# Kernel tuning notes

Measured on AMD Instinct MI355X. Metric: run time of the kernel, lower is better.

The kernel has to match this reference:

```python
import jax, jax.numpy as jnp
import numpy as np

NQ = 8          # n_qubits
NC = 4          # n_cycles of the angle encoder
PI = np.float32(np.pi)
LAYER_QUBITS = [[0, 1, 2, 3, 4, 5, 6, 7], [1, 3, 5, 7]]  # active qubits per conv layer
FINAL_QUBITS = [3, 7]                                    # active after last pooling
CX = jnp.array([[1, 0, 0, 0], [0, 1, 0, 0], [0, 0, 0, 1], [0, 0, 1, 0]], jnp.complex64)


def apply1(psi, U, q):
    """Apply 1-qubit gate U ((2,2) shared or (B,2,2) batched) on qubit q. psi: (B,2,...,2)."""
    psi = jnp.moveaxis(psi, 1 + q, -1)
    if U.ndim == 3:
        psi = jnp.einsum('bij,b...j->b...i', U, psi)
    else:
        psi = jnp.einsum('ij,...j->...i', U, psi)
    return jnp.moveaxis(psi, -1, 1 + q)


def apply2(psi, U, q0, q1):
    """Apply 2-qubit gate U (4,4) on (q0,q1); q0 is the more-significant wire."""
    psi = jnp.moveaxis(psi, (1 + q0, 1 + q1), (-2, -1))
    sh = psi.shape
    psi = jnp.einsum('ij,...j->...i', U, psi.reshape(sh[:-2] + (4,)))
    return jnp.moveaxis(psi.reshape(sh), (-2, -1), (1 + q0, 1 + q1))


def rz_mat(t):
    return jnp.array([[jnp.exp(-0.5j * t), 0.0], [0.0, jnp.exp(0.5j * t)]]).astype(jnp.complex64)


def ry_mat(t):
    c, s = jnp.cos(t / 2), jnp.sin(t / 2)
    return jnp.array([[c, -s], [s, c]]).astype(jnp.complex64)


def crx_mat(t):
    c = jnp.cos(t / 2).astype(jnp.complex64)
    s = jnp.sin(t / 2).astype(jnp.complex64)
    M = jnp.eye(4, dtype=jnp.complex64)
    return M.at[2, 2].set(c).at[3, 3].set(c).at[2, 3].set(-1j * s).at[3, 2].set(-1j * s)


def u3_mat(t, p, l):
    c, s = jnp.cos(t / 2), jnp.sin(t / 2)
    return jnp.array([[c + 0j, -jnp.exp(1j * l) * s],
                      [jnp.exp(1j * p) * s, jnp.exp(1j * (p + l)) * c]]).astype(jnp.complex64)


def expz(psi, q):
    """<Z_q> = P(q=0) - P(q=1)."""
    p = psi.real ** 2 + psi.imag ** 2
    p = jnp.moveaxis(p, 1 + q, 1).reshape(p.shape[0], 2, -1).sum(-1)
    return p[:, 0] - p[:, 1]


def encode(x):
    """Angle-encoding circuit (circuit_builder): NC cycles of RY(x) + CNOT ring."""
    B = x.shape[0]
    psi = jnp.zeros((B, 2 ** NQ), jnp.complex64).at[:, 0].set(1.0).reshape((B,) + (2,) * NQ)
    for c in range(NC):
        ang = x[:, c * NQ:(c + 1) * NQ]
        cc, ss = jnp.cos(ang / 2), jnp.sin(ang / 2)
        for q in range(NQ):
            U = jnp.stack([jnp.stack([cc[:, q], -ss[:, q]], -1),
                           jnp.stack([ss[:, q], cc[:, q]], -1)], -2).astype(jnp.complex64)
            psi = apply1(psi, U, q)
        for q in range(NQ):
            psi = apply2(psi, CX, q, (q + 1) % NQ)
    return psi


def forward(x, rz_p, ry_p, ry2_p, crx_p, u3_p, u3b_p, W1, b1, W2, b2):
    psi0 = encode(x)
    psi1 = psi0  # deepcopy of encoded state for the second feature map
    for layer in range(2):
        aq = LAYER_QUBITS[layer]
        n = len(aq)
        RZp, RYp, RY2p = rz_mat(rz_p[layer]), ry_mat(ry_p[layer]), ry_mat(ry2_p[layer])
        RZm, RZpl = rz_mat(-PI / 2), rz_mat(PI / 2)
        # circuit 1: ZNOTY-style conv blocks, even pairs then odd pairs
        for parity in (0, 1):
            for i in range(parity, n - 1, 2):
                qc, qt = aq[i], aq[i + 1]
                psi0 = apply1(psi0, RZm, qt)
                psi0 = apply2(psi0, CX, qt, qc)
                psi0 = apply1(psi0, RZp, qc)
                psi0 = apply1(psi0, RYp, qt)
                psi0 = apply2(psi0, CX, qc, qt)
                psi0 = apply1(psi0, RY2p, qt)
                psi0 = apply2(psi0, CX, qt, qc)
                psi0 = apply1(psi0, RZpl, qc)
        remain = [aq[i] for i in range(n) if i % 2 == 1]
        U3a = u3_mat(u3_p[layer, 0], u3_p[layer, 1], u3_p[layer, 2])
        for q in remain:
            psi0 = apply1(psi0, U3a, q)
        # circuit 2: CRX conv blocks, even pairs then odd pairs
        CRXp = crx_mat(crx_p[layer])
        for parity in (0, 1):
            for i in range(parity, n - 1, 2):
                psi1 = apply2(psi1, CRXp, aq[i], aq[i + 1])
        U3b = u3_mat(u3b_p[layer, 0], u3b_p[layer, 1], u3b_p[layer, 2])
        for q in remain:
            psi1 = apply1(psi1, U3b, q)
    xv = jnp.stack([expz(psi0, q) for q in FINAL_QUBITS], 1)  # (B,2)
    yv = jnp.stack([expz(psi1, q) for q in FINAL_QUBITS], 1)  # (B,2)
    feat = jnp.concatenate([xv, yv], 1)                       # (B,4)
    h = jnp.tanh(feat @ W1.T + b1)
    return jax.nn.sigmoid(h @ W2.T + b2)


def setup_inputs() -> dict:
    key = jax.random.key(0)
    ks = jax.random.split(key, 12)
    B = 8192
    return {
        'x': jax.random.normal(ks[0], (B, NC * NQ), jnp.float32),
        'rz_p': jax.random.normal(ks[1], (2,), jnp.float32) * 0.5,
        'ry_p': jax.random.normal(ks[2], (2,), jnp.float32) * 0.5,
        'ry2_p': jax.random.normal(ks[3], (2,), jnp.float32) * 0.5,
        'crx_p': jax.random.normal(ks[4], (2,), jnp.float32) * 0.5,
        'u3_p': jax.random.normal(ks[5], (2, 3), jnp.float32) * 0.5,
        'u3b_p': jax.random.normal(ks[6], (2, 3), jnp.float32) * 0.5,
        'W1': jax.random.normal(ks[7], (15, 4), jnp.float32) * 0.4,
        'b1': jax.random.normal(ks[8], (15,), jnp.float32) * 0.1,
        'W2': jax.random.normal(ks[9], (1, 15), jnp.float32) * 0.25,
        'b2': jax.random.normal(ks[10], (1,), jnp.float32) * 0.1,
    }


def reference(x, rz_p, ry_p, ry2_p, crx_p, u3_p, u3b_p, W1, b1, W2, b2):
    return forward(x, rz_p, ry_p, ry2_p, crx_p, u3_p, u3b_p, W1, b1, W2, b2)
```

## Files before the change

kernel.cpp:

```cpp
#include <hip/hip_runtime.h>

#define DEV __device__ __forceinline__

struct C2 { float r, i; };


template<int P>
DEV void ry_cross(float* pr, float* pi, float gc, float gs, int lane) {
  const float cb = ((lane >> P) & 1) ? gs : -gs;
  #pragma unroll
  for (int s = 0; s < 16; ++s) {
    float br = __shfl_xor(pr[s], 1 << P);
    float bi = __shfl_xor(pi[s], 1 << P);
    pr[s] = gc * pr[s] + cb * br;
    pi[s] = gc * pi[s] + cb * bi;
  }
}

template<int M>
DEV void ry_in(float* pr, float* pi, float gc, float gs) {
  #pragma unroll
  for (int s = 0; s < 16; ++s) if (!(s & M)) {
    const int s1 = s | M;
    float ar = pr[s], ai = pi[s], br = pr[s1], bi = pi[s1];
    pr[s]  = gc * ar - gs * br;  pi[s]  = gc * ai - gs * bi;
    pr[s1] = gs * ar + gc * br;  pi[s1] = gs * ai + gc * bi;
  }
}

template<int PC, int PT>
DEV void cx_cc(float* pr, float* pi, int lane) {
  const bool h = (lane >> PC) & 1;
  #pragma unroll
  for (int s = 0; s < 16; ++s) {
    float tr = __shfl_xor(pr[s], 1 << PT);
    float ti = __shfl_xor(pi[s], 1 << PT);
    pr[s] = h ? tr : pr[s];
    pi[s] = h ? ti : pi[s];
  }
}

template<int PC, int MT>
DEV void cx_ci(float* pr, float* pi, int lane) {
  const bool h = (lane >> PC) & 1;
  #pragma unroll
  for (int s = 0; s < 16; ++s) if (!(s & MT)) {
    const int s1 = s | MT;
    float ar = pr[s], br = pr[s1];
    pr[s] = h ? br : ar;  pr[s1] = h ? ar : br;
    float ai = pi[s], bi = pi[s1];
    pi[s] = h ? bi : ai;  pi[s1] = h ? ai : bi;
  }
}

template<int MC, int MT>
DEV void cx_ii(float* pr, float* pi) {
  #pragma unroll
  for (int s = 0; s < 16; ++s) if ((s & MC) && !(s & MT)) {
    const int s1 = s | MT;
    float t;
    t = pr[s]; pr[s] = pr[s1]; pr[s1] = t;
    t = pi[s]; pi[s] = pi[s1]; pi[s1] = t;
  }
}

template<int MC, int PT>
DEV void cx_ic(float* pr, float* pi) {
  #pragma unroll
  for (int s = 0; s < 16; ++s) if (s & MC) {
    pr[s] = __shfl_xor(pr[s], 1 << PT);
    pi[s] = __shfl_xor(pi[s], 1 << PT);
  }
}


template<int PC, int PT>
DEV void u4_cc(float* pr, float* pi, const float* cw, int lay, int lane) {
  const int bc = (lane >> PC) & 1, bt = (lane >> PT) & 1;
  const int r = (bc << 1) | bt;
  const int base = (lay * 16 + r * 4) * 2;
  const float w0r = cw[base + (r ^ 0) * 2], w0i = cw[base + (r ^ 0) * 2 + 1];
  const float w1r = cw[base + (r ^ 1) * 2], w1i = cw[base + (r ^ 1) * 2 + 1];
  const float w2r = cw[base + (r ^ 2) * 2], w2i = cw[base + (r ^ 2) * 2 + 1];
  const float w3r = cw[base + (r ^ 3) * 2], w3i = cw[base + (r ^ 3) * 2 + 1];
  #pragma unroll
  for (int s = 0; s < 16; ++s) {
    float ar = pr[s], ai = pi[s];
    float tr = __shfl_xor(ar, 1 << PT), ti = __shfl_xor(ai, 1 << PT);
    float cr = __shfl_xor(ar, 1 << PC), ci = __shfl_xor(ai, 1 << PC);
    float ur = __shfl_xor(tr, 1 << PC), ui = __shfl_xor(ti, 1 << PC);
    pr[s] = w0r*ar - w0i*ai + w1r*tr - w1i*ti + w2r*cr - w2i*ci + w3r*ur - w3i*ui;
    pi[s] = w0r*ai + w0i*ar + w1r*ti + w1i*tr + w2r*ci + w2i*cr + w3r*ui + w3i*ur;
  }
}

template<int PC, int MT>
DEV void u4_ci(float* pr, float* pi, const float* cw, int lay, int lane) {
  const int bc = (lane >> PC) & 1;
  const int r0 = bc << 1, r1 = r0 | 1;
  const int b0 = (lay * 16 + r0 * 4) * 2;
  const int b1 = (lay * 16 + r1 * 4) * 2;
  const float A0r = cw[b0 + (r0 ^ 0) * 2], A0i = cw[b0 + (r0 ^ 0) * 2 + 1];
  const float A1r = cw[b0 + (r0 ^ 1) * 2], A1i = cw[b0 + (r0 ^ 1) * 2 + 1];
  const float A2r = cw[b0 + (r0 ^ 2) * 2], A2i = cw[b0 + (r0 ^ 2) * 2 + 1];
  const float A3r = cw[b0 + (r0 ^ 3) * 2], A3i = cw[b0 + (r0 ^ 3) * 2 + 1];
  const float B0r = cw[b1 + (r1 ^ 0) * 2], B0i = cw[b1 + (r1 ^ 0) * 2 + 1];
  const float B1r = cw[b1 + (r1 ^ 1) * 2], B1i = cw[b1 + (r1 ^ 1) * 2 + 1];
  const float B2r = cw[b1 + (r1 ^ 2) * 2], B2i = cw[b1 + (r1 ^ 2) * 2 + 1];
  const float B3r = cw[b1 + (r1 ^ 3) * 2], B3i = cw[b1 + (r1 ^ 3) * 2 + 1];
  #pragma unroll
  for (int s = 0; s < 16; ++s) if (!(s & MT)) {
    const int s1 = s | MT;
    float ar = pr[s], ai = pi[s], br = pr[s1], bi = pi[s1];
    float xar = __shfl_xor(ar, 1 << PC), xai = __shfl_xor(ai, 1 << PC);
    float xbr = __shfl_xor(br, 1 << PC), xbi = __shfl_xor(bi, 1 << PC);
    pr[s]  = A0r*ar - A0i*ai + A1r*br - A1i*bi + A2r*xar - A2i*xai + A3r*xbr - A3i*xbi;
    pi[s]  = A0r*ai + A0i*ar + A1r*bi + A1i*br + A2r*xai + A2i*xar + A3r*xbi + A3i*xbr;
    pr[s1] = B0r*br - B0i*bi + B1r*ar - B1i*ai + B2r*xbr - B2i*xbi + B3r*xar - B3i*xai;
    pi[s1] = B0r*bi + B0i*br + B1r*ai + B1i*ar + B2r*xbi + B2i*xbr + B3r*xai + B3i*xar;
  }
}

template<int MC, int MT>
DEV void u4_ii(float* pr, float* pi, const float* cw, int lay) {
  float u[32];
  #pragma unroll
  for (int k = 0; k < 32; ++k) u[k] = cw[lay * 32 + k];
  #pragma unroll
  for (int s = 0; s < 16; ++s) if (!(s & (MC | MT))) {
    const int s0 = s, s1 = s | MT, s2 = s | MC, s3 = s | MC | MT;
    float v0r = pr[s0], v0i = pi[s0], v1r = pr[s1], v1i = pi[s1];
    float v2r = pr[s2], v2i = pi[s2], v3r = pr[s3], v3i = pi[s3];
    float n0r = u[0]*v0r - u[1]*v0i + u[2]*v1r - u[3]*v1i + u[4]*v2r - u[5]*v2i + u[6]*v3r - u[7]*v3i;
    float n0i = u[0]*v0i + u[1]*v0r + u[2]*v1i + u[3]*v1r + u[4]*v2i + u[5]*v2r + u[6]*v3i + u[7]*v3r;
    float n1r = u[8]*v0r - u[9]*v0i + u[10]*v1r - u[11]*v1i + u[12]*v2r - u[13]*v2i + u[14]*v3r - u[15]*v3i;
    float n1i = u[8]*v0i + u[9]*v0r + u[10]*v1i + u[11]*v1r + u[12]*v2i + u[13]*v2r + u[14]*v3i + u[15]*v3r;
    float n2r = u[16]*v0r - u[17]*v0i + u[18]*v1r - u[19]*v1i + u[20]*v2r - u[21]*v2i + u[22]*v3r - u[23]*v3i;
    float n2i = u[16]*v0i + u[17]*v0r + u[18]*v1i + u[19]*v1r + u[20]*v2i + u[21]*v2r + u[22]*v3i + u[23]*v3r;
    float n3r = u[24]*v0r - u[25]*v0i + u[26]*v1r - u[27]*v1i + u[28]*v2r - u[29]*v2i + u[30]*v3r - u[31]*v3i;
    float n3i = u[24]*v0i + u[25]*v0r + u[26]*v1i + u[27]*v1r + u[28]*v2i + u[29]*v2r + u[30]*v3i + u[31]*v3r;
    pr[s0] = n0r; pi[s0] = n0i; pr[s1] = n1r; pi[s1] = n1i;
    pr[s2] = n2r; pi[s2] = n2i; pr[s3] = n3r; pi[s3] = n3i;
  }
}


DEV void u3_make(float t, float p, float l, C2* u) {
  float c = __cosf(0.5f * t), s = __sinf(0.5f * t);
  float cp = __cosf(p), sp = __sinf(p);
  float cl = __cosf(l), sl = __sinf(l);
  float cpl = __cosf(p + l), spl = __sinf(p + l);
  u[0] = C2{c, 0.0f};
  u[1] = C2{-cl * s, -sl * s};
  u[2] = C2{cp * s, sp * s};
  u[3] = C2{cpl * c, spl * c};
}

template<int P>
DEV void u3_cross(float* pr, float* pi, const C2* u, int lane) {
  const bool h = (lane >> P) & 1;
  const float car = h ? u[3].r : u[0].r, cai = h ? u[3].i : u[0].i;
  const float cbr = h ? u[2].r : u[1].r, cbi = h ? u[2].i : u[1].i;
  #pragma unroll
  for (int s = 0; s < 16; ++s) {
    float br = __shfl_xor(pr[s], 1 << P);
    float bi = __shfl_xor(pi[s], 1 << P);
    float ar = pr[s], ai = pi[s];
    pr[s] = car*ar - cai*ai + cbr*br - cbi*bi;
    pi[s] = car*ai + cai*ar + cbr*bi + cbi*br;
  }
}

template<int M>
DEV void u3_in(float* pr, float* pi, const C2* u) {
  #pragma unroll
  for (int s = 0; s < 16; ++s) if (!(s & M)) {
    const int s1 = s | M;
    float ar = pr[s], ai = pi[s], br = pr[s1], bi = pi[s1];
    pr[s]  = u[0].r*ar - u[0].i*ai + u[1].r*br - u[1].i*bi;
    pi[s]  = u[0].r*ai + u[0].i*ar + u[1].r*bi + u[1].i*br;
    pr[s1] = u[2].r*ar - u[2].i*ai + u[3].r*br - u[3].i*bi;
    pi[s1] = u[2].r*ai + u[2].i*ar + u[3].r*bi + u[3].i*br;
  }
}


template<int PC, int PT>
DEV void crx_cc(float* pr, float* pi, float c, float s, int lane) {
  const bool h = (lane >> PC) & 1;
  const float cc = h ? c : 1.0f;
  const float ss = h ? s : 0.0f;
  #pragma unroll
  for (int k = 0; k < 16; ++k) {
    float br = __shfl_xor(pr[k], 1 << PT);
    float bi = __shfl_xor(pi[k], 1 << PT);
    float ar = pr[k], ai = pi[k];
    pr[k] = cc * ar + ss * bi;
    pi[k] = cc * ai - ss * br;
  }
}

template<int PC, int MT>
DEV void crx_ci(float* pr, float* pi, float c, float s, int lane) {
  const bool h = (lane >> PC) & 1;
  const float cc = h ? c : 1.0f;
  const float ss = h ? s : 0.0f;
  #pragma unroll
  for (int k = 0; k < 16; ++k) if (!(k & MT)) {
    const int k1 = k | MT;
    float ar = pr[k], ai = pi[k], br = pr[k1], bi = pi[k1];
    pr[k]  = cc * ar + ss * bi;
    pi[k]  = cc * ai - ss * br;
    pr[k1] = cc * br + ss * ai;
    pi[k1] = cc * bi - ss * ar;
  }
}

template<int MC, int MT>
DEV void crx_ii(float* pr, float* pi, float c, float s) {
  #pragma unroll
  for (int k = 0; k < 16; ++k) if ((k & MC) && !(k & MT)) {
    const int k1 = k | MT;
    float ar = pr[k], ai = pi[k], br = pr[k1], bi = pi[k1];
    pr[k]  = c * ar + s * bi;
    pi[k]  = c * ai - s * br;
    pr[k1] = c * br + s * ai;
    pi[k1] = c * bi - s * ar;
  }
}


DEV void expz37(const float* pr, const float* pi, int lane, float& z3, float& z7) {
  float t3 = 0.0f, t7 = 0.0f;
  #pragma unroll
  for (int s = 0; s < 16; ++s) {
    float p = pr[s] * pr[s] + pi[s] * pi[s];
    t3 += p;
    t7 += (s & 1) ? -p : p;
  }
  t3 = (lane & 1) ? -t3 : t3;
  #pragma unroll
  for (int m = 1; m < 16; m <<= 1) {
    t3 += __shfl_xor(t3, m);
    t7 += __shfl_xor(t7, m);
  }
  z3 = t3; z7 = t7;
}


__global__ __launch_bounds__(256, 2)
void qcnn_kernel(const float* __restrict__ x,
                 const float* __restrict__ rz_p, const float* __restrict__ ry_p,
                 const float* __restrict__ ry2_p, const float* __restrict__ crx_p,
                 const float* __restrict__ u3_p, const float* __restrict__ u3b_p,
                 const float* __restrict__ W1, const float* __restrict__ b1,
                 const float* __restrict__ W2, const float* __restrict__ b2,
                 float* __restrict__ out, int B) {
  __shared__ float cw[64];

  const int tid  = threadIdx.x;
  const int lane = tid & 63;
  const int wave = tid >> 6;
  const int grp  = lane >> 4;
  const int sub  = lane & 15;
  const int elem = blockIdx.x * 16 + wave * 4 + grp;
  const int elemc = elem < B ? elem : (B - 1);

  if (lane < 32) {
    const int lay = lane >> 4, e = lane & 15, i4 = e >> 2, j4 = e & 3;
    const int base = lane & 48;
    const float c45 = 0.70710678118654752f;
    float rz = rz_p[lay], ry = ry_p[lay], ry2 = ry2_p[lay];
    float mr = (i4 == j4) ? c45 : 0.0f;
    float mi = (i4 == j4) ? ((i4 & 1) ? -c45 : c45) : 0.0f;
    { int t = (i4 & 1) ? (i4 ^ 2) : i4; int src = base | (t << 2) | j4;
      mr = __shfl(mr, src); mi = __shfl(mi, src); }
    { float cz = __cosf(0.5f * rz), sz = __sinf(0.5f * rz);
      float di = (i4 & 2) ? sz : -sz;
      float nr = cz * mr - di * mi, ni = cz * mi + di * mr; mr = nr; mi = ni; }
    { float cy = __cosf(0.5f * ry), sy = __sinf(0.5f * ry);
      int src = base | ((i4 ^ 1) << 2) | j4;
      float orr = __shfl(mr, src), oii = __shfl(mi, src);
      float sg = (i4 & 1) ? sy : -sy;
      mr = cy * mr + sg * orr; mi = cy * mi + sg * oii; }
    { int t = (i4 & 2) ? (i4 ^ 1) : i4; int src = base | (t << 2) | j4;
      mr = __shfl(mr, src); mi = __shfl(mi, src); }
    { float cy = __cosf(0.5f * ry2), sy = __sinf(0.5f * ry2);
      int src = base | ((i4 ^ 1) << 2) | j4;
      float orr = __shfl(mr, src), oii = __shfl(mi, src);
      float sg = (i4 & 1) ? sy : -sy;
      mr = cy * mr + sg * orr; mi = cy * mi + sg * oii; }
    { int t = (i4 & 1) ? (i4 ^ 2) : i4; int src = base | (t << 2) | j4;
      mr = __shfl(mr, src); mi = __shfl(mi, src); }
    { float di = (i4 & 2) ? c45 : -c45;
      float nr = c45 * mr - di * mi, ni = c45 * mi + di * mr; mr = nr; mi = ni; }
    cw[(lay * 16 + e) * 2]     = mr;
    cw[(lay * 16 + e) * 2 + 1] = mi;
  }

  float2 aa = ((const float2*)x)[(size_t)elemc * 16 + sub];
  float ch0 = __cosf(0.5f * aa.x), sh0 = __sinf(0.5f * aa.x);
  float ch1 = __cosf(0.5f * aa.y), sh1 = __sinf(0.5f * aa.y);

  float pr[16], pi[16];
  #pragma unroll
  for (int s = 0; s < 16; ++s) { pr[s] = 0.0f; pi[s] = 0.0f; }
  pr[0] = (sub == 0) ? 1.0f : 0.0f;

  #pragma unroll 1
  for (int c = 0; c < 4; ++c) {
    const int sb = lane & 48;
    float gc, gs;
    gc = __shfl(ch0, sb | (c * 4 + 0)); gs = __shfl(sh0, sb | (c * 4 + 0));
    ry_cross<3>(pr, pi, gc, gs, lane);
    gc = __shfl(ch1, sb | (c * 4 + 0)); gs = __shfl(sh1, sb | (c * 4 + 0));
    ry_cross<2>(pr, pi, gc, gs, lane);
    gc = __shfl(ch0, sb | (c * 4 + 1)); gs = __shfl(sh0, sb | (c * 4 + 1));
    ry_cross<1>(pr, pi, gc, gs, lane);
    gc = __shfl(ch1, sb | (c * 4 + 1)); gs = __shfl(sh1, sb | (c * 4 + 1));
    ry_cross<0>(pr, pi, gc, gs, lane);
    gc = __shfl(ch0, sb | (c * 4 + 2)); gs = __shfl(sh0, sb | (c * 4 + 2));
    ry_in<8>(pr, pi, gc, gs);
    gc = __shfl(ch1, sb | (c * 4 + 2)); gs = __shfl(sh1, sb | (c * 4 + 2));
    ry_in<4>(pr, pi, gc, gs);
    gc = __shfl(ch0, sb | (c * 4 + 3)); gs = __shfl(sh0, sb | (c * 4 + 3));
    ry_in<2>(pr, pi, gc, gs);
    gc = __shfl(ch1, sb | (c * 4 + 3)); gs = __shfl(sh1, sb | (c * 4 + 3));
    ry_in<1>(pr, pi, gc, gs);
    cx_cc<3, 2>(pr, pi, lane);
    cx_cc<2, 1>(pr, pi, lane);
    cx_cc<1, 0>(pr, pi, lane);
    cx_ci<0, 8>(pr, pi, lane);
    cx_ii<8, 4>(pr, pi);
    cx_ii<4, 2>(pr, pi);
    cx_ii<2, 1>(pr, pi);
    cx_ic<1, 3>(pr, pi);
  }

  float qr[16], qi[16];
  #pragma unroll
  for (int s = 0; s < 16; ++s) { qr[s] = pr[s]; qi[s] = pi[s]; }

  __syncthreads();

  u4_cc<3, 2>(pr, pi, cw, 0, lane);
  u4_cc<1, 0>(pr, pi, cw, 0, lane);
  u4_ii<8, 4>(pr, pi, cw, 0);
  u4_ii<2, 1>(pr, pi, cw, 0);
  u4_cc<2, 1>(pr, pi, cw, 0, lane);
  u4_ci<0, 8>(pr, pi, cw, 0, lane);
  u4_ii<4, 2>(pr, pi, cw, 0);
  {
    C2 u[4]; u3_make(u3_p[0], u3_p[1], u3_p[2], u);
    u3_cross<2>(pr, pi, u, lane);
    u3_cross<0>(pr, pi, u, lane);
    u3_in<4>(pr, pi, u);
    u3_in<1>(pr, pi, u);
  }
  u4_cc<2, 0>(pr, pi, cw, 1, lane);
  u4_ii<4, 1>(pr, pi, cw, 1);
  u4_ci<0, 4>(pr, pi, cw, 1, lane);
  {
    C2 u[4]; u3_make(u3_p[3], u3_p[4], u3_p[5], u);
    u3_cross<0>(pr, pi, u, lane);
    u3_in<1>(pr, pi, u);
  }

  {
    float t = crx_p[0];
    float cc = __cosf(0.5f * t), ss = __sinf(0.5f * t);
    crx_cc<3, 2>(qr, qi, cc, ss, lane);
    crx_cc<1, 0>(qr, qi, cc, ss, lane);
    crx_ii<8, 4>(qr, qi, cc, ss);
    crx_ii<2, 1>(qr, qi, cc, ss);
    crx_cc<2, 1>(qr, qi, cc, ss, lane);
    crx_ci<0, 8>(qr, qi, cc, ss, lane);
    crx_ii<4, 2>(qr, qi, cc, ss);
  }
  {
    C2 u[4]; u3_make(u3b_p[0], u3b_p[1], u3b_p[2], u);
    u3_cross<2>(qr, qi, u, lane);
    u3_cross<0>(qr, qi, u, lane);
    u3_in<4>(qr, qi, u);
    u3_in<1>(qr, qi, u);
  }
  {
    float t = crx_p[1];
    float cc = __cosf(0.5f * t), ss = __sinf(0.5f * t);
    crx_cc<2, 0>(qr, qi, cc, ss, lane);
    crx_ii<4, 1>(qr, qi, cc, ss);
    crx_ci<0, 4>(qr, qi, cc, ss, lane);
  }
  {
    C2 u[4]; u3_make(u3b_p[3], u3b_p[4], u3b_p[5], u);
    u3_cross<0>(qr, qi, u, lane);
    u3_in<1>(qr, qi, u);
  }

  float f0, f1, f2, f3;
  expz37(pr, pi, lane, f0, f1);
  expz37(qr, qi, lane, f2, f3);

  const int j = (sub < 15) ? sub : 0;
  float acc = W1[j * 4 + 0] * f0 + W1[j * 4 + 1] * f1 +
              W1[j * 4 + 2] * f2 + W1[j * 4 + 3] * f3 + b1[j];
  float e2 = __expf(2.0f * acc);
  float th = (e2 - 1.0f) / (e2 + 1.0f);
  float part = (sub < 15) ? th * W2[j] : 0.0f;
  #pragma unroll
  for (int m = 1; m < 16; m <<= 1) part += __shfl_xor(part, m);

  if (sub == 0 && elem < B) {
    float z = part + b2[0];
    out[elem] = 1.0f / (1.0f + __expf(-z));
  }
}

extern "C" void kernel_launch(void* const* d_in, const int* in_sizes, int n_in,
                              void* d_out, int out_size, void* d_ws, size_t ws_size,
                              hipStream_t stream) {
  (void)n_in; (void)out_size; (void)d_ws; (void)ws_size;
  const float* x     = (const float*)d_in[0];
  const float* rz_p  = (const float*)d_in[1];
  const float* ry_p  = (const float*)d_in[2];
  const float* ry2_p = (const float*)d_in[3];
  const float* crx_p = (const float*)d_in[4];
  const float* u3_p  = (const float*)d_in[5];
  const float* u3b_p = (const float*)d_in[6];
  const float* W1    = (const float*)d_in[7];
  const float* b1    = (const float*)d_in[8];
  const float* W2    = (const float*)d_in[9];
  const float* b2    = (const float*)d_in[10];
  float* out = (float*)d_out;

  const int B = in_sizes[0] / 32;
  const int blocks = (B + 15) / 16;
  qcnn_kernel<<<dim3(blocks), dim3(256), 0, stream>>>(
      x, rz_p, ry_p, ry2_p, crx_p, u3_p, u3b_p, W1, b1, W2, b2, out, B);
}
```

Measured before the change: 133.1 us.

## Absorb CNOT permutations into index tracking and exploit real-valued encoder state

Replaces the explicit CNOT swap passes in the encoder with compile-time parity-based index remapping, so the CNOT ring becomes part of how each RY gate addresses its partners. The first RY layer acting on |0> is computed as a product state in closed form. The encoder keeps only the real part, since RY and CNOT are real, and the imaginary arrays start at zero for the later stages. The two branches now run sequentially, reusing registers, and launch bounds are raised to 4 blocks per CU to cut register pressure. This risks subtle indexing errors in the parity-tracked gate templates.

```diff
diff --git a/kernel.cpp b/kernel.cpp
--- a/kernel.cpp
+++ b/kernel.cpp
@@ -2,243 +2,167 @@
 
 #define DEV __device__ __forceinline__
 
-struct C2 { float r, i; };
-
-
-template<int P>
-DEV void ry_cross(float* pr, float* pi, float gc, float gs, int lane) {
-  const float cb = ((lane >> P) & 1) ? gs : -gs;
+
+DEV int lpar(int lane, int m) { return __builtin_popcount(lane & m) & 1; }
+constexpr int cpar(int v) { return (v ^ (v >> 1) ^ (v >> 2) ^ (v >> 3)) & 1; }
+
+template<int LM, int SM, int LR, int SR>
+DEV void ryr(float* p, float gc, float gs, int lane) {
+  const float sg0 = lpar(lane, LR) ? gs : -gs;
+  const float sg1 = -sg0;
+  if constexpr (LM != 0) {
+    float t[16];
+    #pragma unroll
+    for (int s = 0; s < 16; ++s) t[s] = __shfl_xor(p[s ^ SM], LM);
+    #pragma unroll
+    for (int s = 0; s < 16; ++s)
+      p[s] = gc * p[s] + (cpar(s & SR) ? sg1 : sg0) * t[s];
+  } else {
+    constexpr int LOW = SM & (-SM);
+    #pragma unroll
+    for (int s = 0; s < 16; ++s) if (!(s & LOW)) {
+      const int s1 = s ^ SM;
+      float a = p[s], b = p[s1];
+      float sg = cpar(s & SR) ? sg1 : sg0;
+      p[s]  = gc * a + sg * b;
+      p[s1] = gc * b - sg * a;
+    }
+  }
+}
+
+template<int LM, int SM, int LR, int SR>
+DEV void u3_g(float* pr, float* pi, const float* u, int lane) {
+  const bool hl = lpar(lane, LR);
+  const float d0r = hl ? u[6] : u[0], d0i = hl ? u[7] : u[1];
+  const float o0r = hl ? u[4] : u[2], o0i = hl ? u[5] : u[3];
+  const float d1r = hl ? u[0] : u[6], d1i = hl ? u[1] : u[7];
+  const float o1r = hl ? u[2] : u[4], o1i = hl ? u[3] : u[5];
+  if constexpr (LM != 0) {
+    float tr[16], ti[16];
+    #pragma unroll
+    for (int s = 0; s < 16; ++s) {
+      tr[s] = __shfl_xor(pr[s ^ SM], LM);
+      ti[s] = __shfl_xor(pi[s ^ SM], LM);
+    }
+    #pragma unroll
+    for (int s = 0; s < 16; ++s) {
+      const bool c1 = cpar(s & SR);
+      const float dr = c1 ? d1r : d0r, di = c1 ? d1i : d0i;
+      const float orr = c1 ? o1r : o0r, oi = c1 ? o1i : o0i;
+      float ar = pr[s], ai = pi[s];
+      pr[s] = dr*ar - di*ai + orr*tr[s] - oi*ti[s];
+      pi[s] = dr*ai + di*ar + orr*ti[s] + oi*tr[s];
+    }
+  } else {
+    constexpr int LOW = SM & (-SM);
+    #pragma unroll
+    for (int s = 0; s < 16; ++s) if (!(s & LOW)) {
+      const int s1 = s ^ SM;
+      const bool c1 = cpar(s & SR);
+      const float dAr = c1 ? d1r : d0r, dAi = c1 ? d1i : d0i;
+      const float oAr = c1 ? o1r : o0r, oAi = c1 ? o1i : o0i;
+      const float dBr = c1 ? d0r : d1r, dBi = c1 ? d0i : d1i;
+      const float oBr = c1 ? o0r : o1r, oBi = c1 ? o0i : o1i;
+      float ar = pr[s], ai = pi[s], br = pr[s1], bi = pi[s1];
+      pr[s]  = dAr*ar - dAi*ai + oAr*br - oAi*bi;
+      pi[s]  = dAr*ai + dAi*ar + oAr*bi + oAi*br;
+      pr[s1] = dBr*br - dBi*bi + oBr*ar - oBi*ai;
+      pi[s1] = dBr*bi + dBi*br + oBr*ai + oBi*ar;
+    }
+  }
+}
+
+template<int LMt, int SMt, int LRc, int SRc>
+DEV void crx_g(float* pr, float* pi, float c, float s_, int lane) {
+  const bool hl = lpar(lane, LRc);
+  const float cc0 = hl ? c : 1.0f, ss0 = hl ? s_ : 0.0f;
+  const float cc1 = hl ? 1.0f : c, ss1 = hl ? 0.0f : s_;
+  if constexpr (LMt != 0) {
+    float tr[16], ti[16];
+    #pragma unroll
+    for (int s = 0; s < 16; ++s) {
+      tr[s] = __shfl_xor(pr[s ^ SMt], LMt);
+      ti[s] = __shfl_xor(pi[s ^ SMt], LMt);
+    }
+    #pragma unroll
+    for (int s = 0; s < 16; ++s) {
+      const bool c1 = cpar(s & SRc);
+      const float cc = c1 ? cc1 : cc0, ss = c1 ? ss1 : ss0;
+      float ar = pr[s], ai = pi[s];
+      pr[s] = cc * ar + ss * ti[s];
+      pi[s] = cc * ai - ss * tr[s];
+    }
+  } else {
+    constexpr int LOW = SMt & (-SMt);
+    #pragma unroll
+    for (int s = 0; s < 16; ++s) if (!(s & LOW)) {
+      const int s1 = s ^ SMt;
+      const bool c1 = cpar(s & SRc);
+      const float cc = c1 ? cc1 : cc0, ss = c1 ? ss1 : ss0;
+      float ar = pr[s], ai = pi[s], br = pr[s1], bi = pi[s1];
+      pr[s]  = cc * ar + ss * bi;
+      pi[s]  = cc * ai - ss * br;
+      pr[s1] = cc * br + ss * ai;
+      pi[s1] = cc * bi - ss * ar;
+    }
+  }
+}
+
+#define U4CLASS(Q)                                                            \
+  if constexpr (!(((SRc == 0) && (Q & 2)) || ((SRt == 0) && (Q & 1)))) {      \
+    const int r1 = R ^ Q, r2 = r1 ^ 2;                                        \
+    const float2 wd = w2[r1 * 4 + r1],       wo = w2[r1 * 4 + (r1 ^ 1)];      \
+    const float2 vd = w2[r2 * 4 + r1],       vo = w2[r2 * 4 + (r1 ^ 1)];      \
+    _Pragma("unroll")                                                         \
+    for (int s = 0; s < 16; ++s)                                              \
+      if (((cpar(s & SRc) << 1) | cpar(s & SRt)) == Q) {                      \
+        float ar = pr[s], ai = pi[s], br = tr[s], bi = ti[s];                 \
+        pr[s] = wd.x*ar - wd.y*ai + wo.x*br - wo.y*bi;                        \
+        pi[s] = wd.x*ai + wd.y*ar + wo.x*bi + wo.y*br;                        \
+        tr[s] = vd.x*ar - vd.y*ai + vo.x*br - vo.y*bi;                        \
+        ti[s] = vd.x*ai + vd.y*ar + vo.x*bi + vo.y*br;                        \
+      }                                                                       \
+  }
+
+template<int LMc, int SMc, int LMt, int SMt, int LRc, int SRc, int LRt, int SRt>
+DEV void u4_g(float* pr, float* pi, const float2* w2, int lane) {
+  const int R = (lpar(lane, LRc) << 1) | lpar(lane, LRt);
+  float tr[16], ti[16];
   #pragma unroll
   for (int s = 0; s < 16; ++s) {
-    float br = __shfl_xor(pr[s], 1 << P);
-    float bi = __shfl_xor(pi[s], 1 << P);
-    pr[s] = gc * pr[s] + cb * br;
-    pi[s] = gc * pi[s] + cb * bi;
-  }
-}
-
-template<int M>
-DEV void ry_in(float* pr, float* pi, float gc, float gs) {
-  #pragma unroll
-  for (int s = 0; s < 16; ++s) if (!(s & M)) {
-    const int s1 = s | M;
-    float ar = pr[s], ai = pi[s], br = pr[s1], bi = pi[s1];
-    pr[s]  = gc * ar - gs * br;  pi[s]  = gc * ai - gs * bi;
-    pr[s1] = gs * ar + gc * br;  pi[s1] = gs * ai + gc * bi;
-  }
-}
-
-template<int PC, int PT>
-DEV void cx_cc(float* pr, float* pi, int lane) {
-  const bool h = (lane >> PC) & 1;
+    float vr = pr[s ^ SMt], vi = pi[s ^ SMt];
+    if constexpr (LMt != 0) { vr = __shfl_xor(vr, LMt); vi = __shfl_xor(vi, LMt); }
+    tr[s] = vr; ti[s] = vi;
+  }
+  U4CLASS(0) U4CLASS(1) U4CLASS(2) U4CLASS(3)
   #pragma unroll
   for (int s = 0; s < 16; ++s) {
-    float tr = __shfl_xor(pr[s], 1 << PT);
-    float ti = __shfl_xor(pi[s], 1 << PT);
-    pr[s] = h ? tr : pr[s];
-    pi[s] = h ? ti : pi[s];
-  }
-}
-
-template<int PC, int MT>
-DEV void cx_ci(float* pr, float* pi, int lane) {
-  const bool h = (lane >> PC) & 1;
-  #pragma unroll
-  for (int s = 0; s < 16; ++s) if (!(s & MT)) {
-    const int s1 = s | MT;
-    float ar = pr[s], br = pr[s1];
-    pr[s] = h ? br : ar;  pr[s1] = h ? ar : br;
-    float ai = pi[s], bi = pi[s1];
-    pi[s] = h ? bi : ai;  pi[s1] = h ? ai : bi;
-  }
-}
-
-template<int MC, int MT>
-DEV void cx_ii(float* pr, float* pi) {
-  #pragma unroll
-  for (int s = 0; s < 16; ++s) if ((s & MC) && !(s & MT)) {
-    const int s1 = s | MT;
-    float t;
-    t = pr[s]; pr[s] = pr[s1]; pr[s1] = t;
-    t = pi[s]; pi[s] = pi[s1]; pi[s1] = t;
-  }
-}
-
-template<int MC, int PT>
-DEV void cx_ic(float* pr, float* pi) {
-  #pragma unroll
-  for (int s = 0; s < 16; ++s) if (s & MC) {
-    pr[s] = __shfl_xor(pr[s], 1 << PT);
-    pi[s] = __shfl_xor(pi[s], 1 << PT);
-  }
-}
-
-
-template<int PC, int PT>
-DEV void u4_cc(float* pr, float* pi, const float* cw, int lay, int lane) {
-  const int bc = (lane >> PC) & 1, bt = (lane >> PT) & 1;
-  const int r = (bc << 1) | bt;
-  const int base = (lay * 16 + r * 4) * 2;
-  const float w0r = cw[base + (r ^ 0) * 2], w0i = cw[base + (r ^ 0) * 2 + 1];
-  const float w1r = cw[base + (r ^ 1) * 2], w1i = cw[base + (r ^ 1) * 2 + 1];
-  const float w2r = cw[base + (r ^ 2) * 2], w2i = cw[base + (r ^ 2) * 2 + 1];
-  const float w3r = cw[base + (r ^ 3) * 2], w3i = cw[base + (r ^ 3) * 2 + 1];
-  #pragma unroll
-  for (int s = 0; s < 16; ++s) {
-    float ar = pr[s], ai = pi[s];
-    float tr = __shfl_xor(ar, 1 << PT), ti = __shfl_xor(ai, 1 << PT);
-    float cr = __shfl_xor(ar, 1 << PC), ci = __shfl_xor(ai, 1 << PC);
-    float ur = __shfl_xor(tr, 1 << PC), ui = __shfl_xor(ti, 1 << PC);
-    pr[s] = w0r*ar - w0i*ai + w1r*tr - w1i*ti + w2r*cr - w2i*ci + w3r*ur - w3i*ui;
-    pi[s] = w0r*ai + w0i*ar + w1r*ti + w1i*tr + w2r*ci + w2i*cr + w3r*ui + w3i*ur;
-  }
-}
-
-template<int PC, int MT>
-DEV void u4_ci(float* pr, float* pi, const float* cw, int lay, int lane) {
-  const int bc = (lane >> PC) & 1;
-  const int r0 = bc << 1, r1 = r0 | 1;
-  const int b0 = (lay * 16 + r0 * 4) * 2;
-  const int b1 = (lay * 16 + r1 * 4) * 2;
-  const float A0r = cw[b0 + (r0 ^ 0) * 2], A0i = cw[b0 + (r0 ^ 0) * 2 + 1];
-  const float A1r = cw[b0 + (r0 ^ 1) * 2], A1i = cw[b0 + (r0 ^ 1) * 2 + 1];
-  const float A2r = cw[b0 + (r0 ^ 2) * 2], A2i = cw[b0 + (r0 ^ 2) * 2 + 1];
-  const float A3r = cw[b0 + (r0 ^ 3) * 2], A3i = cw[b0 + (r0 ^ 3) * 2 + 1];
-  const float B0r = cw[b1 + (r1 ^ 0) * 2], B0i = cw[b1 + (r1 ^ 0) * 2 + 1];
-  const float B1r = cw[b1 + (r1 ^ 1) * 2], B1i = cw[b1 + (r1 ^ 1) * 2 + 1];
-  const float B2r = cw[b1 + (r1 ^ 2) * 2], B2i = cw[b1 + (r1 ^ 2) * 2 + 1];
-  const float B3r = cw[b1 + (r1 ^ 3) * 2], B3i = cw[b1 + (r1 ^ 3) * 2 + 1];
-  #pragma unroll
-  for (int s = 0; s < 16; ++s) if (!(s & MT)) {
-    const int s1 = s | MT;
-    float ar = pr[s], ai = pi[s], br = pr[s1], bi = pi[s1];
-    float xar = __shfl_xor(ar, 1 << PC), xai = __shfl_xor(ai, 1 << PC);
-    float xbr = __shfl_xor(br, 1 << PC), xbi = __shfl_xor(bi, 1 << PC);
-    pr[s]  = A0r*ar - A0i*ai + A1r*br - A1i*bi + A2r*xar - A2i*xai + A3r*xbr - A3i*xbi;
-    pi[s]  = A0r*ai + A0i*ar + A1r*bi + A1i*br + A2r*xai + A2i*xar + A3r*xbi + A3i*xbr;
-    pr[s1] = B0r*br - B0i*bi + B1r*ar - B1i*ai + B2r*xbr - B2i*xbi + B3r*xar - B3i*xai;
-    pi[s1] = B0r*bi + B0i*br + B1r*ai + B1i*ar + B2r*xbi + B2i*xbr + B3r*xai + B3i*xar;
-  }
-}
-
-template<int MC, int MT>
-DEV void u4_ii(float* pr, float* pi, const float* cw, int lay) {
-  float u[32];
-  #pragma unroll
-  for (int k = 0; k < 32; ++k) u[k] = cw[lay * 32 + k];
-  #pragma unroll
-  for (int s = 0; s < 16; ++s) if (!(s & (MC | MT))) {
-    const int s0 = s, s1 = s | MT, s2 = s | MC, s3 = s | MC | MT;
-    float v0r = pr[s0], v0i = pi[s0], v1r = pr[s1], v1i = pi[s1];
-    float v2r = pr[s2], v2i = pi[s2], v3r = pr[s3], v3i = pi[s3];
-    float n0r = u[0]*v0r - u[1]*v0i + u[2]*v1r - u[3]*v1i + u[4]*v2r - u[5]*v2i + u[6]*v3r - u[7]*v3i;
-    float n0i = u[0]*v0i + u[1]*v0r + u[2]*v1i + u[3]*v1r + u[4]*v2i + u[5]*v2r + u[6]*v3i + u[7]*v3r;
-    float n1r = u[8]*v0r - u[9]*v0i + u[10]*v1r - u[11]*v1i + u[12]*v2r - u[13]*v2i + u[14]*v3r - u[15]*v3i;
-    float n1i = u[8]*v0i + u[9]*v0r + u[10]*v1i + u[11]*v1r + u[12]*v2i + u[13]*v2r + u[14]*v3i + u[15]*v3r;
-    float n2r = u[16]*v0r - u[17]*v0i + u[18]*v1r - u[19]*v1i + u[20]*v2r - u[21]*v2i + u[22]*v3r - u[23]*v3i;
-    float n2i = u[16]*v0i + u[17]*v0r + u[18]*v1i + u[19]*v1r + u[20]*v2i + u[21]*v2r + u[22]*v3i + u[23]*v3r;
-    float n3r = u[24]*v0r - u[25]*v0i + u[26]*v1r - u[27]*v1i + u[28]*v2r - u[29]*v2i + u[30]*v3r - u[31]*v3i;
-    float n3i = u[24]*v0i + u[25]*v0r + u[26]*v1i + u[27]*v1r + u[28]*v2i + u[29]*v2r + u[30]*v3i + u[31]*v3r;
-    pr[s0] = n0r; pi[s0] = n0i; pr[s1] = n1r; pi[s1] = n1i;
-    pr[s2] = n2r; pi[s2] = n2i; pr[s3] = n3r; pi[s3] = n3i;
-  }
-}
-
-
-DEV void u3_make(float t, float p, float l, C2* u) {
+    float br = tr[s ^ SMc], bi = ti[s ^ SMc];
+    if constexpr (LMc != 0) { br = __shfl_xor(br, LMc); bi = __shfl_xor(bi, LMc); }
+    pr[s] += br; pi[s] += bi;
+  }
+}
+
+DEV void u3_make(float t, float p, float l, float* u) {
   float c = __cosf(0.5f * t), s = __sinf(0.5f * t);
   float cp = __cosf(p), sp = __sinf(p);
   float cl = __cosf(l), sl = __sinf(l);
   float cpl = __cosf(p + l), spl = __sinf(p + l);
-  u[0] = C2{c, 0.0f};
-  u[1] = C2{-cl * s, -sl * s};
-  u[2] = C2{cp * s, sp * s};
-  u[3] = C2{cpl * c, spl * c};
-}
-
-template<int P>
-DEV void u3_cross(float* pr, float* pi, const C2* u, int lane) {
-  const bool h = (lane >> P) & 1;
-  const float car = h ? u[3].r : u[0].r, cai = h ? u[3].i : u[0].i;
-  const float cbr = h ? u[2].r : u[1].r, cbi = h ? u[2].i : u[1].i;
-  #pragma unroll
-  for (int s = 0; s < 16; ++s) {
-    float br = __shfl_xor(pr[s], 1 << P);
-    float bi = __shfl_xor(pi[s], 1 << P);
-    float ar = pr[s], ai = pi[s];
-    pr[s] = car*ar - cai*ai + cbr*br - cbi*bi;
-    pi[s] = car*ai + cai*ar + cbr*bi + cbi*br;
-  }
-}
-
-template<int M>
-DEV void u3_in(float* pr, float* pi, const C2* u) {
-  #pragma unroll
-  for (int s = 0; s < 16; ++s) if (!(s & M)) {
-    const int s1 = s | M;
-    float ar = pr[s], ai = pi[s], br = pr[s1], bi = pi[s1];
-    pr[s]  = u[0].r*ar - u[0].i*ai + u[1].r*br - u[1].i*bi;
-    pi[s]  = u[0].r*ai + u[0].i*ar + u[1].r*bi + u[1].i*br;
-    pr[s1] = u[2].r*ar - u[2].i*ai + u[3].r*br - u[3].i*bi;
-    pi[s1] = u[2].r*ai + u[2].i*ar + u[3].r*bi + u[3].i*br;
-  }
-}
-
-
-template<int PC, int PT>
-DEV void crx_cc(float* pr, float* pi, float c, float s, int lane) {
-  const bool h = (lane >> PC) & 1;
-  const float cc = h ? c : 1.0f;
-  const float ss = h ? s : 0.0f;
-  #pragma unroll
-  for (int k = 0; k < 16; ++k) {
-    float br = __shfl_xor(pr[k], 1 << PT);
-    float bi = __shfl_xor(pi[k], 1 << PT);
-    float ar = pr[k], ai = pi[k];
-    pr[k] = cc * ar + ss * bi;
-    pi[k] = cc * ai - ss * br;
-  }
-}
-
-template<int PC, int MT>
-DEV void crx_ci(float* pr, float* pi, float c, float s, int lane) {
-  const bool h = (lane >> PC) & 1;
-  const float cc = h ? c : 1.0f;
-  const float ss = h ? s : 0.0f;
-  #pragma unroll
-  for (int k = 0; k < 16; ++k) if (!(k & MT)) {
-    const int k1 = k | MT;
-    float ar = pr[k], ai = pi[k], br = pr[k1], bi = pi[k1];
-    pr[k]  = cc * ar + ss * bi;
-    pi[k]  = cc * ai - ss * br;
-    pr[k1] = cc * br + ss * ai;
-    pi[k1] = cc * bi - ss * ar;
-  }
-}
-
-template<int MC, int MT>
-DEV void crx_ii(float* pr, float* pi, float c, float s) {
-  #pragma unroll
-  for (int k = 0; k < 16; ++k) if ((k & MC) && !(k & MT)) {
-    const int k1 = k | MT;
-    float ar = pr[k], ai = pi[k], br = pr[k1], bi = pi[k1];
-    pr[k]  = c * ar + s * bi;
-    pi[k]  = c * ai - s * br;
-    pr[k1] = c * br + s * ai;
-    pi[k1] = c * bi - s * ar;
-  }
-}
-
-
-DEV void expz37(const float* pr, const float* pi, int lane, float& z3, float& z7) {
+  u[0] = c;        u[1] = 0.0f;
+  u[2] = -cl * s;  u[3] = -sl * s;
+  u[4] = cp * s;   u[5] = sp * s;
+  u[6] = cpl * c;  u[7] = spl * c;
+}
+
+DEV void expz_fin(const float* pr, const float* pi, int lane, float& z3, float& z7) {
   float t3 = 0.0f, t7 = 0.0f;
   #pragma unroll
   for (int s = 0; s < 16; ++s) {
     float p = pr[s] * pr[s] + pi[s] * pi[s];
-    t3 += p;
-    t7 += (s & 1) ? -p : p;
-  }
-  t3 = (lane & 1) ? -t3 : t3;
+    t7 += p;
+    t3 += (s & 1) ? -p : p;
+  }
+  if (lpar(lane, 10)) { t3 = -t3; t7 = -t7; }
   #pragma unroll
   for (int m = 1; m < 16; m <<= 1) {
     t3 += __shfl_xor(t3, m);
@@ -248,7 +172,7 @@
 }
 
 
-__global__ __launch_bounds__(256, 2)
+__global__ __launch_bounds__(256, 4)
 void qcnn_kernel(const float* __restrict__ x,
                  const float* __restrict__ rz_p, const float* __restrict__ ry_p,
                  const float* __restrict__ ry2_p, const float* __restrict__ crx_p,
@@ -256,19 +180,20 @@
                  const float* __restrict__ W1, const float* __restrict__ b1,
                  const float* __restrict__ W2, const float* __restrict__ b2,
                  float* __restrict__ out, int B) {
-  __shared__ float cw[64];
+  __shared__ __align__(8) float cw[64];
 
   const int tid  = threadIdx.x;
   const int lane = tid & 63;
   const int wave = tid >> 6;
   const int grp  = lane >> 4;
   const int sub  = lane & 15;
+  const int gb   = lane & 48;
   const int elem = blockIdx.x * 16 + wave * 4 + grp;
   const int elemc = elem < B ? elem : (B - 1);
 
-  if (lane < 32) {
-    const int lay = lane >> 4, e = lane & 15, i4 = e >> 2, j4 = e & 3;
-    const int base = lane & 48;
+  if (tid < 32) {
+    const int lay = tid >> 4, e = tid & 15, i4 = e >> 2, j4 = e & 3;
+    const int base = tid & 48;
     const float c45 = 0.70710678118654752f;
     float rz = rz_p[lay], ry = ry_p[lay], ry2 = ry2_p[lay];
     float mr = (i4 == j4) ? c45 : 0.0f;
@@ -302,104 +227,112 @@
   float ch0 = __cosf(0.5f * aa.x), sh0 = __sinf(0.5f * aa.x);
   float ch1 = __cosf(0.5f * aa.y), sh1 = __sinf(0.5f * aa.y);
 
-  float pr[16], pi[16];
-  #pragma unroll
-  for (int s = 0; s < 16; ++s) { pr[s] = 0.0f; pi[s] = 0.0f; }
-  pr[0] = (sub == 0) ? 1.0f : 0.0f;
-
-  #pragma unroll 1
-  for (int c = 0; c < 4; ++c) {
-    const int sb = lane & 48;
-    float gc, gs;
-    gc = __shfl(ch0, sb | (c * 4 + 0)); gs = __shfl(sh0, sb | (c * 4 + 0));
-    ry_cross<3>(pr, pi, gc, gs, lane);
-    gc = __shfl(ch1, sb | (c * 4 + 0)); gs = __shfl(sh1, sb | (c * 4 + 0));
-    ry_cross<2>(pr, pi, gc, gs, lane);
-    gc = __shfl(ch0, sb | (c * 4 + 1)); gs = __shfl(sh0, sb | (c * 4 + 1));
-    ry_cross<1>(pr, pi, gc, gs, lane);
-    gc = __shfl(ch1, sb | (c * 4 + 1)); gs = __shfl(sh1, sb | (c * 4 + 1));
-    ry_cross<0>(pr, pi, gc, gs, lane);
-    gc = __shfl(ch0, sb | (c * 4 + 2)); gs = __shfl(sh0, sb | (c * 4 + 2));
-    ry_in<8>(pr, pi, gc, gs);
-    gc = __shfl(ch1, sb | (c * 4 + 2)); gs = __shfl(sh1, sb | (c * 4 + 2));
-    ry_in<4>(pr, pi, gc, gs);
-    gc = __shfl(ch0, sb | (c * 4 + 3)); gs = __shfl(sh0, sb | (c * 4 + 3));
-    ry_in<2>(pr, pi, gc, gs);
-    gc = __shfl(ch1, sb | (c * 4 + 3)); gs = __shfl(sh1, sb | (c * 4 + 3));
-    ry_in<1>(pr, pi, gc, gs);
-    cx_cc<3, 2>(pr, pi, lane);
-    cx_cc<2, 1>(pr, pi, lane);
-    cx_cc<1, 0>(pr, pi, lane);
-    cx_ci<0, 8>(pr, pi, lane);
-    cx_ii<8, 4>(pr, pi);
-    cx_ii<4, 2>(pr, pi);
-    cx_ii<2, 1>(pr, pi);
-    cx_ic<1, 3>(pr, pi);
-  }
-
-  float qr[16], qi[16];
-  #pragma unroll
-  for (int s = 0; s < 16; ++s) { qr[s] = pr[s]; qi[s] = pi[s]; }
+  float cq[8], sq[8];
+  #pragma unroll
+  for (int q = 0; q < 8; ++q) {
+    cq[q] = __shfl((q & 1) ? ch1 : ch0, gb | (q >> 1));
+    sq[q] = __shfl((q & 1) ? sh1 : sh0, gb | (q >> 1));
+  }
+
+  float p[16];
+  {
+    float g = ((sub & 8) ? sq[0] : cq[0]) * ((sub & 4) ? sq[2] : cq[2]) *
+              ((sub & 2) ? sq[4] : cq[4]) * ((sub & 1) ? sq[6] : cq[6]);
+    float h13[4] = {cq[1]*cq[3], cq[1]*sq[3], sq[1]*cq[3], sq[1]*sq[3]};
+    float h57[4] = {cq[5]*cq[7], cq[5]*sq[7], sq[5]*cq[7], sq[5]*sq[7]};
+    #pragma unroll
+    for (int i = 0; i < 4; ++i) h13[i] *= g;
+    #pragma unroll
+    for (int s = 0; s < 16; ++s) p[s] = h13[s >> 2] * h57[s & 3];
+  }
+
+  #define ENC(k, LM, SM, LR, SR) {                                  \
+    float gc = __shfl(((k) & 1) ? ch1 : ch0, gb | ((k) >> 1));      \
+    float gs = __shfl(((k) & 1) ? sh1 : sh0, gb | ((k) >> 1));      \
+    ryr<LM, SM, LR, SR>(p, gc, gs, lane); }
+
+  ENC(8,  8,8, 7,15)  ENC(9,  4,8, 8,8)   ENC(10, 4,4, 12,8)  ENC(11, 2,4, 12,12)
+  ENC(12, 2,2, 14,12) ENC(13, 1,2, 14,14) ENC(14, 1,1, 15,14) ENC(15, 8,9, 15,15)
+  ENC(16, 12,0, 8,15) ENC(17, 0,12, 15,7) ENC(18, 6,0, 3,15)  ENC(19, 0,6, 15,3)
+  ENC(20, 3,0, 1,15)  ENC(21, 0,3, 15,1)  ENC(22, 9,8, 0,15)  ENC(23, 4,9, 15,0)
+  ENC(24, 12,12, 2,10) ENC(25, 6,12, 7,8) ENC(26, 6,6, 4,7)   ENC(27, 3,6, 11,4)
+  ENC(28, 3,3, 10,11)  ENC(29, 9,11, 5,10) ENC(30, 13,1, 5,5) ENC(31, 8,5, 10,5)
+  #undef ENC
+
+  float enc[16];
+  #pragma unroll
+  for (int s = 0; s < 16; ++s) enc[s] = p[s];
 
   __syncthreads();
-
-  u4_cc<3, 2>(pr, pi, cw, 0, lane);
-  u4_cc<1, 0>(pr, pi, cw, 0, lane);
-  u4_ii<8, 4>(pr, pi, cw, 0);
-  u4_ii<2, 1>(pr, pi, cw, 0);
-  u4_cc<2, 1>(pr, pi, cw, 0, lane);
-  u4_ci<0, 8>(pr, pi, cw, 0, lane);
-  u4_ii<4, 2>(pr, pi, cw, 0);
-  {
-    C2 u[4]; u3_make(u3_p[0], u3_p[1], u3_p[2], u);
-    u3_cross<2>(pr, pi, u, lane);
-    u3_cross<0>(pr, pi, u, lane);
-    u3_in<4>(pr, pi, u);
-    u3_in<1>(pr, pi, u);
-  }
-  u4_cc<2, 0>(pr, pi, cw, 1, lane);
-  u4_ii<4, 1>(pr, pi, cw, 1);
-  u4_ci<0, 4>(pr, pi, cw, 1, lane);
-  {
-    C2 u[4]; u3_make(u3_p[3], u3_p[4], u3_p[5], u);
-    u3_cross<0>(pr, pi, u, lane);
-    u3_in<1>(pr, pi, u);
-  }
+  const float2* w0 = (const float2*)cw;
+  const float2* w1 = ((const float2*)cw) + 16;
+
+  float pi_[16];
+  #pragma unroll
+  for (int s = 0; s < 16; ++s) pi_[s] = 0.0f;
+
+  u4_g<10,0,  0,10, 8,10, 5,2 >(p, pi_, w0, lane);
+  u4_g<5,0,   0,5,  1,5,  10,1>(p, pi_, w0, lane);
+  u4_g<10,8,  4,10, 0,10, 5,0 >(p, pi_, w0, lane);
+  u4_g<5,4,   2,5,  0,5,  10,0>(p, pi_, w0, lane);
+  u4_g<0,10,  5,0,  5,2,  1,5 >(p, pi_, w0, lane);
+  u4_g<0,5,   10,8, 10,1, 0,10>(p, pi_, w0, lane);
+  u4_g<4,10,  5,4,  5,0,  0,5 >(p, pi_, w0, lane);
+  {
+    float ua[8]; u3_make(u3_p[0], u3_p[1], u3_p[2], ua);
+    u3_g<0,10, 5,2 >(p, pi_, ua, lane);
+    u3_g<0,5,  10,1>(p, pi_, ua, lane);
+    u3_g<4,10, 5,0 >(p, pi_, ua, lane);
+    u3_g<2,5,  10,0>(p, pi_, ua, lane);
+  }
+  u4_g<0,10,  0,5,  5,2,  10,1>(p, pi_, w1, lane);
+  u4_g<4,10,  2,5,  5,0,  10,0>(p, pi_, w1, lane);
+  u4_g<0,5,   4,10, 10,1, 5,0 >(p, pi_, w1, lane);
+  {
+    float ua[8]; u3_make(u3_p[3], u3_p[4], u3_p[5], ua);
+    u3_g<0,5,  10,1>(p, pi_, ua, lane);
+    u3_g<2,5,  10,0>(p, pi_, ua, lane);
+  }
+
+  float f0, f1;
+  expz_fin(p, pi_, lane, f0, f1);
+
+  #pragma unroll
+  for (int s = 0; s < 16; ++s) { p[s] = enc[s]; pi_[s] = 0.0f; }
 
   {
     float t = crx_p[0];
     float cc = __cosf(0.5f * t), ss = __sinf(0.5f * t);
-    crx_cc<3, 2>(qr, qi, cc, ss, lane);
-    crx_cc<1, 0>(qr, qi, cc, ss, lane);
-    crx_ii<8, 4>(qr, qi, cc, ss);
-    crx_ii<2, 1>(qr, qi, cc, ss);
-    crx_cc<2, 1>(qr, qi, cc, ss, lane);
-    crx_ci<0, 8>(qr, qi, cc, ss, lane);
-    crx_ii<4, 2>(qr, qi, cc, ss);
-  }
-  {
-    C2 u[4]; u3_make(u3b_p[0], u3b_p[1], u3b_p[2], u);
-    u3_cross<2>(qr, qi, u, lane);
-    u3_cross<0>(qr, qi, u, lane);
-    u3_in<4>(qr, qi, u);
-    u3_in<1>(qr, qi, u);
+    crx_g<0,10, 8,10>(p, pi_, cc, ss, lane);
+    crx_g<0,5,  1,5 >(p, pi_, cc, ss, lane);
+    crx_g<4,10, 0,10>(p, pi_, cc, ss, lane);
+    crx_g<2,5,  0,5 >(p, pi_, cc, ss, lane);
+    crx_g<5,0,  5,2 >(p, pi_, cc, ss, lane);
+    crx_g<10,8, 10,1>(p, pi_, cc, ss, lane);
+    crx_g<5,4,  5,0 >(p, pi_, cc, ss, lane);
+  }
+  {
+    float ub[8]; u3_make(u3b_p[0], u3b_p[1], u3b_p[2], ub);
+    u3_g<0,10, 5,2 >(p, pi_, ub, lane);
+    u3_g<0,5,  10,1>(p, pi_, ub, lane);
+    u3_g<4,10, 5,0 >(p, pi_, ub, lane);
+    u3_g<2,5,  10,0>(p, pi_, ub, lane);
   }
   {
     float t = crx_p[1];
     float cc = __cosf(0.5f * t), ss = __sinf(0.5f * t);
-    crx_cc<2, 0>(qr, qi, cc, ss, lane);
-    crx_ii<4, 1>(qr, qi, cc, ss);
-    crx_ci<0, 4>(qr, qi, cc, ss, lane);
-  }
-  {
-    C2 u[4]; u3_make(u3b_p[3], u3b_p[4], u3b_p[5], u);
-    u3_cross<0>(qr, qi, u, lane);
-    u3_in<1>(qr, qi, u);
-  }
-
-  float f0, f1, f2, f3;
-  expz37(pr, pi, lane, f0, f1);
-  expz37(qr, qi, lane, f2, f3);
+    crx_g<0,5,  5,2 >(p, pi_, cc, ss, lane);
+    crx_g<2,5,  5,0 >(p, pi_, cc, ss, lane);
+    crx_g<4,10, 10,1>(p, pi_, cc, ss, lane);
+  }
+  {
+    float ub[8]; u3_make(u3b_p[3], u3b_p[4], u3b_p[5], ub);
+    u3_g<0,5,  10,1>(p, pi_, ub, lane);
+    u3_g<2,5,  10,0>(p, pi_, ub, lane);
+  }
+
+  float f2, f3;
+  expz_fin(p, pi_, lane, f2, f3);
 
   const int j = (sub < 15) ? sub : 0;
   float acc = W1[j * 4 + 0] * f0 + W1[j * 4 + 1] * f1 +
```

After: 200.2 us. 50.4% more time.
